# Performance work log

Hardware: AMD Instinct MI355X
Metric: run time of the kernel (lower is better)

The kernel has to match this reference:

```python
import jax, jax.numpy as jnp
import numpy as np

N = 1000000
SH_COEFFS = 16  # (sh_degree+1)^2 with sh_degree=3
H = 256
W = 256
K_RENDER = 1000  # module renders min(1000, N) front-most-by-descending-depth splats


def setup_inputs():
    key = jax.random.key(0)
    k = jax.random.split(key, 5)
    positions = jax.random.normal(k[0], (N, 3), jnp.float32) * 0.1
    scales = jnp.ones((N, 3), jnp.float32) * 0.01
    rotations = jax.random.normal(k[1], (N, 4), jnp.float32)
    colors = jax.random.normal(k[2], (N, 3), jnp.float32)
    opacity = jnp.ones((N, 1), jnp.float32) * 0.1
    colors_sh = jax.random.normal(k[3], (N, SH_COEFFS, 3), jnp.float32) * 0.001
    # realistic pinhole camera: fx=fy=500, cx=cy=128, translation z=2 so depths>0
    camera_matrix = jnp.array([[500.0, 0.0, 128.0, 0.0],
                               [0.0, 500.0, 128.0, 0.0],
                               [0.0, 0.0, 1.0, 2.0]], jnp.float32)
    camera_position = jax.random.normal(k[4], (3,), jnp.float32) * 0.1
    return {"positions": positions, "scales": scales, "rotations": rotations,
            "colors": colors, "opacity": opacity, "colors_sh": colors_sh,
            "camera_matrix": camera_matrix, "camera_position": camera_position,
            "image_height": H, "image_width": W}


def _covariance(scales, rotations):
    # Sigma = R S S^T R^T, quaternion -> rotation matrix
    q = rotations / jnp.linalg.norm(rotations, axis=-1, keepdims=True)
    w, x, y, z = q[:, 0], q[:, 1], q[:, 2], q[:, 3]
    R = jnp.stack([
        jnp.stack([1 - 2 * (y * y + z * z), 2 * (x * y - w * z), 2 * (x * z + w * y)], -1),
        jnp.stack([2 * (x * y + w * z), 1 - 2 * (x * x + z * z), 2 * (y * z - w * x)], -1),
        jnp.stack([2 * (x * z - w * y), 2 * (y * z + w * x), 1 - 2 * (x * x + y * y)], -1)], -2)  # [N,3,3]
    s2 = jnp.clip(scales, 1e-7, None) ** 2
    return jnp.einsum('nij,nj,nkj->nik', R, s2, R)


def _sh_bases(d):
    x, y, z = d[:, 0], d[:, 1], d[:, 2]
    return jnp.stack([
        jnp.full_like(x, 0.28209479177387814),
        -0.48860251190291987 * y, 0.48860251190291987 * z, -0.48860251190291987 * x,
        1.0925484305920792 * x * y, -1.0925484305920792 * y * z,
        0.31539156525252005 * (2 * z * z - x * x - y * y),
        -1.0925484305920792 * x * z, 0.5462742152960396 * (x * x - y * y)], -1)  # [N,9]


def _forward(positions, scales, rotations, colors, opacity, colors_sh,
             camera_matrix, camera_position, image_height, image_width):
    cov3d = _covariance(jnp.exp(scales), rotations)  # [N,3,3]
    # perspective projection
    pos_h = jnp.concatenate([positions, jnp.ones((positions.shape[0], 1), positions.dtype)], -1)
    proj = pos_h @ camera_matrix.T  # [N,3]
    depths = proj[:, 2]
    pos2d = proj[:, :2] / (depths[:, None] + 1e-7)
    fx, fy = camera_matrix[0, 0], camera_matrix[1, 1]
    zero = jnp.zeros_like(depths)
    J = jnp.stack([
        jnp.stack([fx / depths, zero, -fx * pos2d[:, 0] / depths], -1),
        jnp.stack([zero, fy / depths, -fy * pos2d[:, 1] / depths], -1)], -2)  # [N,2,3]
    cov2d = jnp.einsum('nij,njk,nlk->nil', J, cov3d, J)  # [N,2,2]
    # view-dependent color via SH (only first 9 bases, as in the torch loop)
    vd = positions - camera_position[None]
    vd = vd / jnp.linalg.norm(vd, axis=-1, keepdims=True)
    sh = _sh_bases(vd)
    col = jax.nn.sigmoid(colors + jnp.einsum('nkc,nk->nc', colors_sh[:, :sh.shape[-1]], sh))
    op = jax.nn.sigmoid(opacity[:, 0])
    # depth sort descending, keep first K_RENDER (matches min(1000, N) loop)
    order = jnp.argsort(-depths)[:K_RENDER]
    mu_s, cov_s, col_s, op_s = pos2d[order], cov2d[order], col[order], op[order]
    ys = jnp.arange(image_height, dtype=jnp.float32)
    xs = jnp.arange(image_width, dtype=jnp.float32)
    yy, xx = jnp.meshgrid(ys, xs, indexing='ij')
    px = xx.reshape(-1)
    py = yy.reshape(-1)  # [P]
    P = image_height * image_width

    def step(carry, g):
        rendered, acc = carry
        mu, cv, c, o = g
        # 2x2 inverse of (cov + 1e-6 I), closed form
        a = cv[0, 0] + 1e-6
        b = cv[0, 1]
        cc = cv[1, 0]
        d = cv[1, 1] + 1e-6
        det = a * d - b * cc
        dx = px - mu[0]
        dy = py - mu[1]
        qv = (d * dx * dx - (b + cc) * dx * dy + a * dy * dy) / det
        alpha = o * jnp.exp(-0.5 * qv)           # [P]
        contrib = (1.0 - acc) * alpha            # front-to-back compositing
        rendered = rendered + contrib[:, None] * c
        acc = acc + contrib
        return (rendered, acc), None

    init = (jnp.zeros((P, 3), jnp.float32), jnp.zeros((P,), jnp.float32))
    (rendered, _), _ = jax.lax.scan(step, init, (mu_s, cov_s, col_s, op_s))
    return rendered.reshape(image_height, image_width, 3)


def reference(positions, scales, rotations, colors, opacity, colors_sh,
              camera_matrix, camera_position, image_height, image_width):
    return _forward(positions, scales, rotations, colors, opacity, colors_sh,
                    camera_matrix, camera_position, image_height, image_width)
```

## Files before the change

### kernel.cpp

```cpp
#include <hip/hip_runtime.h>
#include <stdint.h>

typedef uint32_t u32;
typedef uint64_t u64;

#define KREN 1000
#define NBLK 256
#define NTHR 1024
#define TOT (NBLK * NTHR)
#define CAND0_CAP 16384
#define CAND_CAP 4096
#define GSTRIDE 12
#define SEGN 16
#define PXT 4

__device__ __forceinline__ u32 fkey(float f) {
  u32 b = __float_as_uint(f);
  return (b & 0x80000000u) ? ~b : (b | 0x80000000u);
}

__device__ __forceinline__ void grid_sync(u32* bar) {
  __syncthreads();
  if (threadIdx.x == 0) {
    u32 gen = __hip_atomic_load(&bar[1], __ATOMIC_RELAXED, __HIP_MEMORY_SCOPE_AGENT);
    u32 arr = __hip_atomic_fetch_add(&bar[0], 1u, __ATOMIC_RELEASE, __HIP_MEMORY_SCOPE_AGENT);
    if (arr == NBLK - 1) {
      __hip_atomic_store(&bar[0], 0u, __ATOMIC_RELAXED, __HIP_MEMORY_SCOPE_AGENT);
      __hip_atomic_store(&bar[1], gen + 1u, __ATOMIC_RELEASE, __HIP_MEMORY_SCOPE_AGENT);
    } else {
      while (__hip_atomic_load(&bar[1], __ATOMIC_RELAXED, __HIP_MEMORY_SCOPE_AGENT) == gen)
        __builtin_amdgcn_s_sleep(4);
    }
    __builtin_amdgcn_fence(__ATOMIC_ACQUIRE, "agent");
  }
  __syncthreads();
}

__device__ __forceinline__ void pick_scan(const u32* __restrict__ hist, u32 K,
                                          u32* lds, int* bin_out, u32* Krem_out) {
  int tid = threadIdx.x;
  u32 hv[4];
  u32 s = 0;
#pragma unroll
  for (int k = 0; k < 4; ++k) { hv[k] = hist[tid * 4 + k]; s += hv[k]; }
  lds[tid] = s;
  __syncthreads();
  for (int d = 1; d < NTHR; d <<= 1) {
    u32 v = lds[tid] + ((tid + d < NTHR) ? lds[tid + d] : 0u);
    __syncthreads();
    lds[tid] = v;
    __syncthreads();
  }
  u32 inc = lds[tid];
  u32 above = (tid < NTHR - 1) ? lds[tid + 1] : 0u;
  if (above < K && inc >= K) {
    u32 cum = above;
    for (int k = 3; k >= 0; --k) {
      cum += hv[k];
      if (cum >= K) {
        lds[NTHR] = (u32)(tid * 4 + k);
        lds[NTHR + 1] = K - (cum - hv[k]);
        break;
      }
    }
  }
  __syncthreads();
  *bin_out = (int)lds[NTHR];
  *Krem_out = lds[NTHR + 1];
  __syncthreads();
}

__global__ __launch_bounds__(NTHR) void k_fused(
    const float* __restrict__ pos, const float* __restrict__ scales,
    const float* __restrict__ rot, const float* __restrict__ colors,
    const float* __restrict__ opac, const float* __restrict__ csh,
    const float* __restrict__ cam, const float* __restrict__ campos,
    u32* __restrict__ keys, u64* __restrict__ cand0, u64* __restrict__ cand,
    float* __restrict__ gauss, u32* __restrict__ hist1, u32* __restrict__ hist2,
    u32* __restrict__ state, u32* __restrict__ bar, float* __restrict__ out,
    int N, int shstride) {
  __shared__ u64 smem[8192];
  u32* hl = (u32*)smem;
  int tid = threadIdx.x, bid = blockIdx.x;
  int gtid = bid * NTHR + tid;
  int lane = tid & 63;

  for (int i = tid; i < 4096; i += NTHR) hl[i] = 0;
  __syncthreads();
  {
    float c8 = cam[8], c9 = cam[9], c10 = cam[10], c11 = cam[11];
    for (int i = gtid; i < N; i += TOT) {
      float x = pos[3 * i], y = pos[3 * i + 1], z = pos[3 * i + 2];
      u32 mk = fkey(c8 * x + c9 * y + c10 * z + c11);
      keys[i] = mk;
      u32 bin = mk >> 20;
      u64 todo = __ballot(true);
      while (todo) {
        int leader = __ffsll((unsigned long long)todo) - 1;
        u32 lbin = __shfl(bin, leader, 64);
        u64 same = __ballot(bin == lbin);
        if (lane == leader) atomicAdd(&hl[lbin], (u32)__popcll(same & todo));
        todo &= ~same;
      }
    }
  }
  __syncthreads();
  for (int i = tid; i < 4096; i += NTHR) {
    u32 v = hl[i];
    if (v) atomicAdd(&hist1[i], v);
  }
  grid_sync(bar);

  int bin1; u32 K1;
  pick_scan(hist1, (u32)KREN, hl, &bin1, &K1);
  u32 pref = (u32)bin1;
  for (int i = tid; i < 4096; i += NTHR) hl[i] = 0;
  __syncthreads();
  for (int i = gtid; i < N; i += TOT) {
    u32 k = keys[i];
    bool m = (k >> 20) == pref;
    if (m) atomicAdd(&hl[(k >> 8) & 4095u], 1u);
    u64 bm = __ballot(m);
    if (bm) {
      u32 base;
      int leader = __ffsll((unsigned long long)bm) - 1;
      if (lane == leader) base = atomicAdd(&state[1], (u32)__popcll(bm));
      base = __shfl(base, leader, 64);
      if (m) {
        u32 p = base + (u32)__popcll(bm & ((1ull << lane) - 1ull));
        if (p < CAND0_CAP) cand0[p] = (((u64)(~k)) << 32) | (u32)i;
      }
    }
  }
  __syncthreads();
  for (int i = tid; i < 4096; i += NTHR) {
    u32 v = hl[i];
    if (v) atomicAdd(&hist2[i], v);
  }
  grid_sync(bar);

  int bin2; u32 K2;
  pick_scan(hist2, K1, hl, &bin2, &K2);
  {
    u32 Thi = ~((pref << 20) | (((u32)bin2) << 8));
    int M1 = (int)state[1];
    if (M1 > CAND0_CAP) M1 = CAND0_CAP;
    for (int i = gtid; i < M1; i += TOT) {
      u64 e = cand0[i];
      if ((u32)(e >> 32) <= Thi) {
        u32 p = atomicAdd(&state[0], 1u);
        if (p < CAND_CAP) cand[p] = e;
      }
    }
  }
  grid_sync(bar);

  {
    u64* sc = smem;
    int M = (int)state[0];
    if (M > CAND_CAP) M = CAND_CAP;
    for (int i = tid; i < M; i += NTHR) sc[i] = cand[i];
    __syncthreads();
    int w = tid >> 6;
    int c = bid * 16 + w;
    if (c < M) {
      u64 mine = sc[c];
      int cnt = 0;
      int JJ = (M + 63) >> 6;
      for (int jj = 0; jj < JJ; ++jj) {
        int j = lane + (jj << 6);
        if (j < M && sc[j] < mine) ++cnt;
      }
#pragma unroll
      for (int d = 32; d; d >>= 1) cnt += __shfl_xor(cnt, d, 64);
      int r = cnt;
      if (r < KREN && lane == 0) {
        int g = (int)(u32)(mine & 0xffffffffu);
        float x = pos[3 * g], y = pos[3 * g + 1], z = pos[3 * g + 2];
        float c0 = cam[0], c1 = cam[1], c2 = cam[2], c3 = cam[3];
        float c4 = cam[4], c5 = cam[5], c6 = cam[6], c7 = cam[7];
        float c8 = cam[8], c9 = cam[9], c10 = cam[10], c11 = cam[11];
        float dep = c8 * x + c9 * y + c10 * z + c11;
        float invd = 1.0f / (dep + 1e-7f);
        float p2x = (c0 * x + c1 * y + c2 * z + c3) * invd;
        float p2y = (c4 * x + c5 * y + c6 * z + c7) * invd;
        float qw = rot[4 * g], qx = rot[4 * g + 1], qy = rot[4 * g + 2], qz = rot[4 * g + 3];
        float qn = rsqrtf(qw * qw + qx * qx + qy * qy + qz * qz);
        qw *= qn; qx *= qn; qy *= qn; qz *= qn;
        float r00 = 1.f - 2.f * (qy * qy + qz * qz), r01 = 2.f * (qx * qy - qw * qz), r02 = 2.f * (qx * qz + qw * qy);
        float r10 = 2.f * (qx * qy + qw * qz), r11 = 1.f - 2.f * (qx * qx + qz * qz), r12 = 2.f * (qy * qz - qw * qx);
        float r20 = 2.f * (qx * qz - qw * qy), r21 = 2.f * (qy * qz + qw * qx), r22 = 1.f - 2.f * (qx * qx + qy * qy);
        float e0 = fmaxf(expf(scales[3 * g]), 1e-7f);
        float e1 = fmaxf(expf(scales[3 * g + 1]), 1e-7f);
        float e2 = fmaxf(expf(scales[3 * g + 2]), 1e-7f);
        float v0 = e0 * e0, v1 = e1 * e1, v2 = e2 * e2;
        float C00 = r00 * r00 * v0 + r01 * r01 * v1 + r02 * r02 * v2;
        float C01 = r00 * r10 * v0 + r01 * r11 * v1 + r02 * r12 * v2;
        float C02 = r00 * r20 * v0 + r01 * r21 * v1 + r02 * r22 * v2;
        float C11 = r10 * r10 * v0 + r11 * r11 * v1 + r12 * r12 * v2;
        float C12 = r10 * r20 * v0 + r11 * r21 * v1 + r12 * r22 * v2;
        float C22 = r20 * r20 * v0 + r21 * r21 * v1 + r22 * r22 * v2;
        float fx = c0, fy = c5;
        float jd = 1.0f / dep;
        float j0 = fx * jd, j2 = -fx * p2x * jd, j4 = fy * jd, j5 = -fy * p2y * jd;
        float u0x = j0 * C00 + j2 * C02;
        float u0y = j0 * C01 + j2 * C12;
        float u0z = j0 * C02 + j2 * C22;
        float u1y = j4 * C11 + j5 * C12;
        float u1z = j4 * C12 + j5 * C22;
        float a = u0x * j0 + u0z * j2 + 1e-6f;
        float b = u0y * j4 + u0z * j5;
        float d2 = u1y * j4 + u1z * j5 + 1e-6f;
        float det = a * d2 - b * b;
        float idet = 1.0f / det;
        const float L = 1.4426950408889634f;
        float Aq = -0.5f * L * d2 * idet;
        float Bq = L * b * idet;
        float Cq = -0.5f * L * a * idet;
        float vx = x - campos[0], vy = y - campos[1], vz = z - campos[2];
        float vn = rsqrtf(vx * vx + vy * vy + vz * vz);
        vx *= vn; vy *= vn; vz *= vn;
        float sh[9];
        sh[0] = 0.28209479177387814f;
        sh[1] = -0.48860251190291987f * vy;
        sh[2] = 0.48860251190291987f * vz;
        sh[3] = -0.48860251190291987f * vx;
        sh[4] = 1.0925484305920792f * vx * vy;
        sh[5] = -1.0925484305920792f * vy * vz;
        sh[6] = 0.31539156525252005f * (2.f * vz * vz - vx * vx - vy * vy);
        sh[7] = -1.0925484305920792f * vx * vz;
        sh[8] = 0.5462742152960396f * (vx * vx - vy * vy);
        float col[3];
        for (int c2 = 0; c2 < 3; ++c2) {
          float accv = colors[3 * g + c2];
          for (int k2 = 0; k2 < 9; ++k2) accv += sh[k2] * csh[(size_t)g * shstride + 3 * k2 + c2];
          col[c2] = 1.0f / (1.0f + __expf(-accv));
        }
        float op = 1.0f / (1.0f + __expf(-opac[g]));
        float* G = gauss + r * GSTRIDE;
        G[0] = p2x; G[1] = p2y; G[2] = Aq; G[3] = Bq; G[4] = Cq;
        G[5] = op;  G[6] = col[0]; G[7] = col[1]; G[8] = col[2];
        G[9] = 0.f; G[10] = 0.f; G[11] = 0.f;
      }
    }
  }
  grid_sync(bar);

  {
    float* gs = (float*)smem;
    float4* g4s = (float4*)smem;
    const float4* g4 = (const float4*)gauss;
    for (int i = tid; i < 3000; i += NTHR) g4s[i] = g4[i];
    __syncthreads();
    int grp = tid & 63;
    int seg = tid >> 6;
    float pxf = (float)(grp * 4);
    float pyf = (float)bid;
    float cr0 = 0.f, cr1 = 0.f, cr2 = 0.f, cr3 = 0.f;
    float cg0 = 0.f, cg1 = 0.f, cg2 = 0.f, cg3 = 0.f;
    float cb0 = 0.f, cb1 = 0.f, cb2 = 0.f, cb3 = 0.f;
    float ac0 = 0.f, ac1 = 0.f, ac2 = 0.f, ac3 = 0.f;
    int gbeg = (seg * KREN) / SEGN, gend = ((seg + 1) * KREN) / SEGN;
    for (int k = gbeg; k < gend; ++k) {
      const float4* Gp = (const float4*)(gs + k * GSTRIDE);
      float4 g0 = Gp[0];
      float4 g1 = Gp[1];
      float g2x = gs[k * GSTRIDE + 8];
      float A = g0.z, B = g0.w, C = g1.x, op = g1.y;
      float dx = pxf - g0.x, dy = pyf - g0.y;
      float q0 = (A * dx + B * dy) * dx + C * dy * dy;
      float u = 2.f * A * dx + B * dy;
      float q1 = q0 + u + A;
      float q2 = q0 + 2.f * u + 4.f * A;
      float q3 = q0 + 3.f * u + 9.f * A;
      float e0 = op * exp2f(q0), e1 = op * exp2f(q1);
      float e2 = op * exp2f(q2), e3 = op * exp2f(q3);
      float w0 = (1.f - ac0) * e0, w1 = (1.f - ac1) * e1;
      float w2 = (1.f - ac2) * e2, w3 = (1.f - ac3) * e3;
      cr0 += w0 * g1.z; cg0 += w0 * g1.w; cb0 += w0 * g2x; ac0 += w0;
      cr1 += w1 * g1.z; cg1 += w1 * g1.w; cb1 += w1 * g2x; ac1 += w1;
      cr2 += w2 * g1.z; cg2 += w2 * g1.w; cb2 += w2 * g2x; ac2 += w2;
      cr3 += w3 * g1.z; cg3 += w3 * g1.w; cb3 += w3 * g2x; ac3 += w3;
    }
    __syncthreads();
    float4* comb = (float4*)smem;
    int base = seg * 256 + grp * 4;
    comb[base + 0] = make_float4(cr0, cg0, cb0, 1.f - ac0);
    comb[base + 1] = make_float4(cr1, cg1, cb1, 1.f - ac1);
    comb[base + 2] = make_float4(cr2, cg2, cb2, 1.f - ac2);
    comb[base + 3] = make_float4(cr3, cg3, cb3, 1.f - ac3);
    __syncthreads();
    if (tid < 256) {
      int px = tid;
      float R = 0.f, Gc = 0.f, Bc = 0.f, T = 1.f;
#pragma unroll
      for (int s2 = 0; s2 < SEGN; ++s2) {
        float4 cv = comb[s2 * 256 + px];
        R += T * cv.x; Gc += T * cv.y; Bc += T * cv.z;
        T *= cv.w;
      }
      int p = bid * 256 + px;
      out[3 * p + 0] = R;
      out[3 * p + 1] = Gc;
      out[3 * p + 2] = Bc;
    }
  }
}

extern "C" void kernel_launch(void* const* d_in, const int* in_sizes, int n_in,
                              void* d_out, int out_size, void* d_ws, size_t ws_size,
                              hipStream_t stream) {
  const float* positions = (const float*)d_in[0];
  const float* scales    = (const float*)d_in[1];
  const float* rotations = (const float*)d_in[2];
  const float* colors    = (const float*)d_in[3];
  const float* opacity   = (const float*)d_in[4];
  const float* colors_sh = (const float*)d_in[5];
  const float* cam       = (const float*)d_in[6];
  const float* campos    = (const float*)d_in[7];
  int N = in_sizes[0] / 3;
  int shstride = in_sizes[5] / N;

  char* ws = (char*)d_ws;
  u32* keys    = (u32*)ws;
  u64* cand0   = (u64*)(ws + 4194304);
  u64* cand    = (u64*)(ws + 4325376);
  float* gauss = (float*)(ws + 4358144);
  char* zr     = ws + 4407296;
  u32* hist1   = (u32*)zr;
  u32* hist2   = (u32*)(zr + 16384);
  u32* state   = (u32*)(zr + 32768);
  u32* bar     = (u32*)(zr + 33024);
  float* out   = (float*)d_out;

  hipMemsetAsync(zr, 0, 33280, stream);

  void* args[] = {(void*)&positions, (void*)&scales, (void*)&rotations, (void*)&colors,
                  (void*)&opacity, (void*)&colors_sh, (void*)&cam, (void*)&campos,
                  (void*)&keys, (void*)&cand0, (void*)&cand, (void*)&gauss,
                  (void*)&hist1, (void*)&hist2, (void*)&state, (void*)&bar,
                  (void*)&out, (void*)&N, (void*)&shstride};
  hipLaunchCooperativeKernel((const void*)k_fused, dim3(NBLK), dim3(NTHR), args, 0, stream);
}
```

Baseline: 450.2 us.

## Split cooperative fused kernel into five stream-ordered kernels

Replaces the single cooperative kernel and its software grid barriers with five separate launches (key/histogram, refine histogram and candidate gather, threshold filter, rank and preprocess, render), each with its own grid and block size. The candidate filter now uses wave-aggregated atomics instead of per-thread atomics, and the first-stage bin and remaining count are passed between kernels through workspace state. This is meant to remove the cost of spinning grid barriers and cooperative launch limits, and to let each phase use a suitable occupancy. In exchange it adds several kernel launch gaps and re-reads intermediate data from global memory.

```diff
diff --git a/kernel.cpp b/kernel.cpp
--- a/kernel.cpp
+++ b/kernel.cpp
@@ -5,118 +5,101 @@
 typedef uint64_t u64;
 
 #define KREN 1000
-#define NBLK 256
-#define NTHR 1024
-#define TOT (NBLK * NTHR)
 #define CAND0_CAP 16384
 #define CAND_CAP 4096
 #define GSTRIDE 12
 #define SEGN 16
-#define PXT 4
+#define P0_BLK 512
+#define P1_BLK 512
+#define P2_BLK 32
+#define P3_BLK 1024
 
 __device__ __forceinline__ u32 fkey(float f) {
   u32 b = __float_as_uint(f);
   return (b & 0x80000000u) ? ~b : (b | 0x80000000u);
 }
 
-__device__ __forceinline__ void grid_sync(u32* bar) {
-  __syncthreads();
-  if (threadIdx.x == 0) {
-    u32 gen = __hip_atomic_load(&bar[1], __ATOMIC_RELAXED, __HIP_MEMORY_SCOPE_AGENT);
-    u32 arr = __hip_atomic_fetch_add(&bar[0], 1u, __ATOMIC_RELEASE, __HIP_MEMORY_SCOPE_AGENT);
-    if (arr == NBLK - 1) {
-      __hip_atomic_store(&bar[0], 0u, __ATOMIC_RELAXED, __HIP_MEMORY_SCOPE_AGENT);
-      __hip_atomic_store(&bar[1], gen + 1u, __ATOMIC_RELEASE, __HIP_MEMORY_SCOPE_AGENT);
-    } else {
-      while (__hip_atomic_load(&bar[1], __ATOMIC_RELAXED, __HIP_MEMORY_SCOPE_AGENT) == gen)
-        __builtin_amdgcn_s_sleep(4);
-    }
-    __builtin_amdgcn_fence(__ATOMIC_ACQUIRE, "agent");
-  }
-  __syncthreads();
-}
-
-__device__ __forceinline__ void pick_scan(const u32* __restrict__ hist, u32 K,
-                                          u32* lds, int* bin_out, u32* Krem_out) {
+__device__ __forceinline__ void pick_scan256(const u32* __restrict__ hist, u32 K,
+                                             u32* lds, int* bin_out, u32* Krem_out) {
   int tid = threadIdx.x;
-  u32 hv[4];
+  u32 hv[16];
   u32 s = 0;
 #pragma unroll
-  for (int k = 0; k < 4; ++k) { hv[k] = hist[tid * 4 + k]; s += hv[k]; }
+  for (int k = 0; k < 16; ++k) { hv[k] = hist[tid * 16 + k]; s += hv[k]; }
   lds[tid] = s;
   __syncthreads();
-  for (int d = 1; d < NTHR; d <<= 1) {
-    u32 v = lds[tid] + ((tid + d < NTHR) ? lds[tid + d] : 0u);
+  for (int d = 1; d < 256; d <<= 1) {
+    u32 v = lds[tid] + ((tid + d < 256) ? lds[tid + d] : 0u);
     __syncthreads();
     lds[tid] = v;
     __syncthreads();
   }
   u32 inc = lds[tid];
-  u32 above = (tid < NTHR - 1) ? lds[tid + 1] : 0u;
+  u32 above = (tid < 255) ? lds[tid + 1] : 0u;
   if (above < K && inc >= K) {
     u32 cum = above;
-    for (int k = 3; k >= 0; --k) {
+    for (int k = 15; k >= 0; --k) {
       cum += hv[k];
       if (cum >= K) {
-        lds[NTHR] = (u32)(tid * 4 + k);
-        lds[NTHR + 1] = K - (cum - hv[k]);
+        lds[256] = (u32)(tid * 16 + k);
+        lds[257] = K - (cum - hv[k]);
         break;
       }
     }
   }
   __syncthreads();
-  *bin_out = (int)lds[NTHR];
-  *Krem_out = lds[NTHR + 1];
-  __syncthreads();
-}
-
-__global__ __launch_bounds__(NTHR) void k_fused(
-    const float* __restrict__ pos, const float* __restrict__ scales,
-    const float* __restrict__ rot, const float* __restrict__ colors,
-    const float* __restrict__ opac, const float* __restrict__ csh,
-    const float* __restrict__ cam, const float* __restrict__ campos,
-    u32* __restrict__ keys, u64* __restrict__ cand0, u64* __restrict__ cand,
-    float* __restrict__ gauss, u32* __restrict__ hist1, u32* __restrict__ hist2,
-    u32* __restrict__ state, u32* __restrict__ bar, float* __restrict__ out,
-    int N, int shstride) {
-  __shared__ u64 smem[8192];
-  u32* hl = (u32*)smem;
-  int tid = threadIdx.x, bid = blockIdx.x;
-  int gtid = bid * NTHR + tid;
+  *bin_out = (int)lds[256];
+  *Krem_out = lds[257];
+  __syncthreads();
+}
+
+__global__ __launch_bounds__(256) void k_p0(const float* __restrict__ pos,
+                                            const float* __restrict__ cam,
+                                            u32* __restrict__ keys,
+                                            u32* __restrict__ hist1, int N) {
+  __shared__ u32 hl[4096];
+  int tid = threadIdx.x;
   int lane = tid & 63;
-
-  for (int i = tid; i < 4096; i += NTHR) hl[i] = 0;
-  __syncthreads();
-  {
-    float c8 = cam[8], c9 = cam[9], c10 = cam[10], c11 = cam[11];
-    for (int i = gtid; i < N; i += TOT) {
-      float x = pos[3 * i], y = pos[3 * i + 1], z = pos[3 * i + 2];
-      u32 mk = fkey(c8 * x + c9 * y + c10 * z + c11);
-      keys[i] = mk;
-      u32 bin = mk >> 20;
-      u64 todo = __ballot(true);
-      while (todo) {
-        int leader = __ffsll((unsigned long long)todo) - 1;
-        u32 lbin = __shfl(bin, leader, 64);
-        u64 same = __ballot(bin == lbin);
-        if (lane == leader) atomicAdd(&hl[lbin], (u32)__popcll(same & todo));
-        todo &= ~same;
-      }
-    }
-  }
-  __syncthreads();
-  for (int i = tid; i < 4096; i += NTHR) {
+  for (int i = tid; i < 4096; i += 256) hl[i] = 0;
+  __syncthreads();
+  float c8 = cam[8], c9 = cam[9], c10 = cam[10], c11 = cam[11];
+  for (int i = blockIdx.x * 256 + tid; i < N; i += P0_BLK * 256) {
+    float x = pos[3 * i], y = pos[3 * i + 1], z = pos[3 * i + 2];
+    u32 mk = fkey(c8 * x + c9 * y + c10 * z + c11);
+    keys[i] = mk;
+    u32 bin = mk >> 20;
+    u64 todo = __ballot(true);
+    while (todo) {
+      int leader = __ffsll((unsigned long long)todo) - 1;
+      u32 lbin = __shfl(bin, leader, 64);
+      u64 same = __ballot(bin == lbin);
+      if (lane == leader) atomicAdd(&hl[lbin], (u32)__popcll(same & todo));
+      todo &= ~same;
+    }
+  }
+  __syncthreads();
+  for (int i = tid; i < 4096; i += 256) {
     u32 v = hl[i];
     if (v) atomicAdd(&hist1[i], v);
   }
-  grid_sync(bar);
-
+}
+
+__global__ __launch_bounds__(256) void k_p1(const u32* __restrict__ keys,
+                                            const u32* __restrict__ hist1,
+                                            u32* __restrict__ hist2,
+                                            u64* __restrict__ cand0,
+                                            u32* __restrict__ state, int N) {
+  __shared__ u32 hl[4096];
+  __shared__ u32 sl[258];
+  int tid = threadIdx.x;
+  int lane = tid & 63;
   int bin1; u32 K1;
-  pick_scan(hist1, (u32)KREN, hl, &bin1, &K1);
+  pick_scan256(hist1, (u32)KREN, sl, &bin1, &K1);
+  if (tid == 0) { state[4] = K1; state[5] = (u32)bin1; }
   u32 pref = (u32)bin1;
-  for (int i = tid; i < 4096; i += NTHR) hl[i] = 0;
-  __syncthreads();
-  for (int i = gtid; i < N; i += TOT) {
+  for (int i = tid; i < 4096; i += 256) hl[i] = 0;
+  __syncthreads();
+  for (int i = blockIdx.x * 256 + tid; i < N; i += P1_BLK * 256) {
     u32 k = keys[i];
     bool m = (k >> 20) == pref;
     if (m) atomicAdd(&hl[(k >> 8) & 4095u], 1u);
@@ -133,177 +116,199 @@
     }
   }
   __syncthreads();
-  for (int i = tid; i < 4096; i += NTHR) {
+  for (int i = tid; i < 4096; i += 256) {
     u32 v = hl[i];
     if (v) atomicAdd(&hist2[i], v);
   }
-  grid_sync(bar);
-
+}
+
+__global__ __launch_bounds__(256) void k_p2(const u64* __restrict__ cand0,
+                                            const u32* __restrict__ hist2,
+                                            u64* __restrict__ cand,
+                                            u32* __restrict__ state) {
+  __shared__ u32 sl[258];
+  int tid = threadIdx.x;
+  int lane = tid & 63;
+  u32 K1 = state[4];
+  u32 pref = state[5];
   int bin2; u32 K2;
-  pick_scan(hist2, K1, hl, &bin2, &K2);
-  {
-    u32 Thi = ~((pref << 20) | (((u32)bin2) << 8));
-    int M1 = (int)state[1];
-    if (M1 > CAND0_CAP) M1 = CAND0_CAP;
-    for (int i = gtid; i < M1; i += TOT) {
-      u64 e = cand0[i];
-      if ((u32)(e >> 32) <= Thi) {
-        u32 p = atomicAdd(&state[0], 1u);
+  pick_scan256(hist2, K1, sl, &bin2, &K2);
+  u32 Thi = ~((pref << 20) | (((u32)bin2) << 8));
+  int M1 = (int)state[1];
+  if (M1 > CAND0_CAP) M1 = CAND0_CAP;
+  for (int i = blockIdx.x * 256 + tid; i < M1; i += P2_BLK * 256) {
+    u64 e = cand0[i];
+    bool m = (u32)(e >> 32) <= Thi;
+    u64 bm = __ballot(m);
+    if (bm) {
+      u32 base;
+      int leader = __ffsll((unsigned long long)bm) - 1;
+      if (lane == leader) base = atomicAdd(&state[0], (u32)__popcll(bm));
+      base = __shfl(base, leader, 64);
+      if (m) {
+        u32 p = base + (u32)__popcll(bm & ((1ull << lane) - 1ull));
         if (p < CAND_CAP) cand[p] = e;
       }
     }
   }
-  grid_sync(bar);
-
-  {
-    u64* sc = smem;
-    int M = (int)state[0];
-    if (M > CAND_CAP) M = CAND_CAP;
-    for (int i = tid; i < M; i += NTHR) sc[i] = cand[i];
-    __syncthreads();
-    int w = tid >> 6;
-    int c = bid * 16 + w;
-    if (c < M) {
-      u64 mine = sc[c];
-      int cnt = 0;
-      int JJ = (M + 63) >> 6;
-      for (int jj = 0; jj < JJ; ++jj) {
-        int j = lane + (jj << 6);
-        if (j < M && sc[j] < mine) ++cnt;
-      }
+}
+
+__global__ __launch_bounds__(256) void k_p3(
+    const u64* __restrict__ cand, const u32* __restrict__ state,
+    const float* __restrict__ pos, const float* __restrict__ scales,
+    const float* __restrict__ rot, const float* __restrict__ colors,
+    const float* __restrict__ opac, const float* __restrict__ csh,
+    const float* __restrict__ cam, const float* __restrict__ campos,
+    float* __restrict__ gauss, int shstride) {
+  __shared__ u64 sc[CAND_CAP];
+  int tid = threadIdx.x, bid = blockIdx.x;
+  int lane = tid & 63;
+  int M = (int)state[0];
+  if (M > CAND_CAP) M = CAND_CAP;
+  if (bid * 4 >= M) return;
+  for (int i = tid; i < M; i += 256) sc[i] = cand[i];
+  __syncthreads();
+  int c = bid * 4 + (tid >> 6);
+  if (c >= M) return;
+  u64 mine = sc[c];
+  int cnt = 0;
+  int JJ = (M + 63) >> 6;
+  for (int jj = 0; jj < JJ; ++jj) {
+    int j = lane + (jj << 6);
+    if (j < M && sc[j] < mine) ++cnt;
+  }
 #pragma unroll
-      for (int d = 32; d; d >>= 1) cnt += __shfl_xor(cnt, d, 64);
-      int r = cnt;
-      if (r < KREN && lane == 0) {
-        int g = (int)(u32)(mine & 0xffffffffu);
-        float x = pos[3 * g], y = pos[3 * g + 1], z = pos[3 * g + 2];
-        float c0 = cam[0], c1 = cam[1], c2 = cam[2], c3 = cam[3];
-        float c4 = cam[4], c5 = cam[5], c6 = cam[6], c7 = cam[7];
-        float c8 = cam[8], c9 = cam[9], c10 = cam[10], c11 = cam[11];
-        float dep = c8 * x + c9 * y + c10 * z + c11;
-        float invd = 1.0f / (dep + 1e-7f);
-        float p2x = (c0 * x + c1 * y + c2 * z + c3) * invd;
-        float p2y = (c4 * x + c5 * y + c6 * z + c7) * invd;
-        float qw = rot[4 * g], qx = rot[4 * g + 1], qy = rot[4 * g + 2], qz = rot[4 * g + 3];
-        float qn = rsqrtf(qw * qw + qx * qx + qy * qy + qz * qz);
-        qw *= qn; qx *= qn; qy *= qn; qz *= qn;
-        float r00 = 1.f - 2.f * (qy * qy + qz * qz), r01 = 2.f * (qx * qy - qw * qz), r02 = 2.f * (qx * qz + qw * qy);
-        float r10 = 2.f * (qx * qy + qw * qz), r11 = 1.f - 2.f * (qx * qx + qz * qz), r12 = 2.f * (qy * qz - qw * qx);
-        float r20 = 2.f * (qx * qz - qw * qy), r21 = 2.f * (qy * qz + qw * qx), r22 = 1.f - 2.f * (qx * qx + qy * qy);
-        float e0 = fmaxf(expf(scales[3 * g]), 1e-7f);
-        float e1 = fmaxf(expf(scales[3 * g + 1]), 1e-7f);
-        float e2 = fmaxf(expf(scales[3 * g + 2]), 1e-7f);
-        float v0 = e0 * e0, v1 = e1 * e1, v2 = e2 * e2;
-        float C00 = r00 * r00 * v0 + r01 * r01 * v1 + r02 * r02 * v2;
-        float C01 = r00 * r10 * v0 + r01 * r11 * v1 + r02 * r12 * v2;
-        float C02 = r00 * r20 * v0 + r01 * r21 * v1 + r02 * r22 * v2;
-        float C11 = r10 * r10 * v0 + r11 * r11 * v1 + r12 * r12 * v2;
-        float C12 = r10 * r20 * v0 + r11 * r21 * v1 + r12 * r22 * v2;
-        float C22 = r20 * r20 * v0 + r21 * r21 * v1 + r22 * r22 * v2;
-        float fx = c0, fy = c5;
-        float jd = 1.0f / dep;
-        float j0 = fx * jd, j2 = -fx * p2x * jd, j4 = fy * jd, j5 = -fy * p2y * jd;
-        float u0x = j0 * C00 + j2 * C02;
-        float u0y = j0 * C01 + j2 * C12;
-        float u0z = j0 * C02 + j2 * C22;
-        float u1y = j4 * C11 + j5 * C12;
-        float u1z = j4 * C12 + j5 * C22;
-        float a = u0x * j0 + u0z * j2 + 1e-6f;
-        float b = u0y * j4 + u0z * j5;
-        float d2 = u1y * j4 + u1z * j5 + 1e-6f;
-        float det = a * d2 - b * b;
-        float idet = 1.0f / det;
-        const float L = 1.4426950408889634f;
-        float Aq = -0.5f * L * d2 * idet;
-        float Bq = L * b * idet;
-        float Cq = -0.5f * L * a * idet;
-        float vx = x - campos[0], vy = y - campos[1], vz = z - campos[2];
-        float vn = rsqrtf(vx * vx + vy * vy + vz * vz);
-        vx *= vn; vy *= vn; vz *= vn;
-        float sh[9];
-        sh[0] = 0.28209479177387814f;
-        sh[1] = -0.48860251190291987f * vy;
-        sh[2] = 0.48860251190291987f * vz;
-        sh[3] = -0.48860251190291987f * vx;
-        sh[4] = 1.0925484305920792f * vx * vy;
-        sh[5] = -1.0925484305920792f * vy * vz;
-        sh[6] = 0.31539156525252005f * (2.f * vz * vz - vx * vx - vy * vy);
-        sh[7] = -1.0925484305920792f * vx * vz;
-        sh[8] = 0.5462742152960396f * (vx * vx - vy * vy);
-        float col[3];
-        for (int c2 = 0; c2 < 3; ++c2) {
-          float accv = colors[3 * g + c2];
-          for (int k2 = 0; k2 < 9; ++k2) accv += sh[k2] * csh[(size_t)g * shstride + 3 * k2 + c2];
-          col[c2] = 1.0f / (1.0f + __expf(-accv));
-        }
-        float op = 1.0f / (1.0f + __expf(-opac[g]));
-        float* G = gauss + r * GSTRIDE;
-        G[0] = p2x; G[1] = p2y; G[2] = Aq; G[3] = Bq; G[4] = Cq;
-        G[5] = op;  G[6] = col[0]; G[7] = col[1]; G[8] = col[2];
-        G[9] = 0.f; G[10] = 0.f; G[11] = 0.f;
-      }
-    }
-  }
-  grid_sync(bar);
-
-  {
-    float* gs = (float*)smem;
-    float4* g4s = (float4*)smem;
-    const float4* g4 = (const float4*)gauss;
-    for (int i = tid; i < 3000; i += NTHR) g4s[i] = g4[i];
-    __syncthreads();
-    int grp = tid & 63;
-    int seg = tid >> 6;
-    float pxf = (float)(grp * 4);
-    float pyf = (float)bid;
-    float cr0 = 0.f, cr1 = 0.f, cr2 = 0.f, cr3 = 0.f;
-    float cg0 = 0.f, cg1 = 0.f, cg2 = 0.f, cg3 = 0.f;
-    float cb0 = 0.f, cb1 = 0.f, cb2 = 0.f, cb3 = 0.f;
-    float ac0 = 0.f, ac1 = 0.f, ac2 = 0.f, ac3 = 0.f;
-    int gbeg = (seg * KREN) / SEGN, gend = ((seg + 1) * KREN) / SEGN;
-    for (int k = gbeg; k < gend; ++k) {
-      const float4* Gp = (const float4*)(gs + k * GSTRIDE);
-      float4 g0 = Gp[0];
-      float4 g1 = Gp[1];
-      float g2x = gs[k * GSTRIDE + 8];
-      float A = g0.z, B = g0.w, C = g1.x, op = g1.y;
-      float dx = pxf - g0.x, dy = pyf - g0.y;
-      float q0 = (A * dx + B * dy) * dx + C * dy * dy;
-      float u = 2.f * A * dx + B * dy;
-      float q1 = q0 + u + A;
-      float q2 = q0 + 2.f * u + 4.f * A;
-      float q3 = q0 + 3.f * u + 9.f * A;
-      float e0 = op * exp2f(q0), e1 = op * exp2f(q1);
-      float e2 = op * exp2f(q2), e3 = op * exp2f(q3);
-      float w0 = (1.f - ac0) * e0, w1 = (1.f - ac1) * e1;
-      float w2 = (1.f - ac2) * e2, w3 = (1.f - ac3) * e3;
-      cr0 += w0 * g1.z; cg0 += w0 * g1.w; cb0 += w0 * g2x; ac0 += w0;
-      cr1 += w1 * g1.z; cg1 += w1 * g1.w; cb1 += w1 * g2x; ac1 += w1;
-      cr2 += w2 * g1.z; cg2 += w2 * g1.w; cb2 += w2 * g2x; ac2 += w2;
-      cr3 += w3 * g1.z; cg3 += w3 * g1.w; cb3 += w3 * g2x; ac3 += w3;
-    }
-    __syncthreads();
-    float4* comb = (float4*)smem;
-    int base = seg * 256 + grp * 4;
-    comb[base + 0] = make_float4(cr0, cg0, cb0, 1.f - ac0);
-    comb[base + 1] = make_float4(cr1, cg1, cb1, 1.f - ac1);
-    comb[base + 2] = make_float4(cr2, cg2, cb2, 1.f - ac2);
-    comb[base + 3] = make_float4(cr3, cg3, cb3, 1.f - ac3);
-    __syncthreads();
-    if (tid < 256) {
-      int px = tid;
-      float R = 0.f, Gc = 0.f, Bc = 0.f, T = 1.f;
+  for (int d = 32; d; d >>= 1) cnt += __shfl_xor(cnt, d, 64);
+  int r = cnt;
+  if (r >= KREN || lane != 0) return;
+  int g = (int)(u32)(mine & 0xffffffffu);
+  float x = pos[3 * g], y = pos[3 * g + 1], z = pos[3 * g + 2];
+  float c0 = cam[0], c1 = cam[1], c2 = cam[2], c3 = cam[3];
+  float c4 = cam[4], c5 = cam[5], c6 = cam[6], c7 = cam[7];
+  float c8 = cam[8], c9 = cam[9], c10 = cam[10], c11 = cam[11];
+  float dep = c8 * x + c9 * y + c10 * z + c11;
+  float invd = 1.0f / (dep + 1e-7f);
+  float p2x = (c0 * x + c1 * y + c2 * z + c3) * invd;
+  float p2y = (c4 * x + c5 * y + c6 * z + c7) * invd;
+  float qw = rot[4 * g], qx = rot[4 * g + 1], qy = rot[4 * g + 2], qz = rot[4 * g + 3];
+  float qn = rsqrtf(qw * qw + qx * qx + qy * qy + qz * qz);
+  qw *= qn; qx *= qn; qy *= qn; qz *= qn;
+  float r00 = 1.f - 2.f * (qy * qy + qz * qz), r01 = 2.f * (qx * qy - qw * qz), r02 = 2.f * (qx * qz + qw * qy);
+  float r10 = 2.f * (qx * qy + qw * qz), r11 = 1.f - 2.f * (qx * qx + qz * qz), r12 = 2.f * (qy * qz - qw * qx);
+  float r20 = 2.f * (qx * qz - qw * qy), r21 = 2.f * (qy * qz + qw * qx), r22 = 1.f - 2.f * (qx * qx + qy * qy);
+  float e0 = fmaxf(expf(scales[3 * g]), 1e-7f);
+  float e1 = fmaxf(expf(scales[3 * g + 1]), 1e-7f);
+  float e2 = fmaxf(expf(scales[3 * g + 2]), 1e-7f);
+  float v0 = e0 * e0, v1 = e1 * e1, v2 = e2 * e2;
+  float C00 = r00 * r00 * v0 + r01 * r01 * v1 + r02 * r02 * v2;
+  float C01 = r00 * r10 * v0 + r01 * r11 * v1 + r02 * r12 * v2;
+  float C02 = r00 * r20 * v0 + r01 * r21 * v1 + r02 * r22 * v2;
+  float C11 = r10 * r10 * v0 + r11 * r11 * v1 + r12 * r12 * v2;
+  float C12 = r10 * r20 * v0 + r11 * r21 * v1 + r12 * r22 * v2;
+  float C22 = r20 * r20 * v0 + r21 * r21 * v1 + r22 * r22 * v2;
+  float fx = c0, fy = c5;
+  float jd = 1.0f / dep;
+  float j0 = fx * jd, j2 = -fx * p2x * jd, j4 = fy * jd, j5 = -fy * p2y * jd;
+  float u0x = j0 * C00 + j2 * C02;
+  float u0y = j0 * C01 + j2 * C12;
+  float u0z = j0 * C02 + j2 * C22;
+  float u1y = j4 * C11 + j5 * C12;
+  float u1z = j4 * C12 + j5 * C22;
+  float a = u0x * j0 + u0z * j2 + 1e-6f;
+  float b = u0y * j4 + u0z * j5;
+  float d2 = u1y * j4 + u1z * j5 + 1e-6f;
+  float det = a * d2 - b * b;
+  float idet = 1.0f / det;
+  const float L = 1.4426950408889634f;
+  float Aq = -0.5f * L * d2 * idet;
+  float Bq = L * b * idet;
+  float Cq = -0.5f * L * a * idet;
+  float vx = x - campos[0], vy = y - campos[1], vz = z - campos[2];
+  float vn = rsqrtf(vx * vx + vy * vy + vz * vz);
+  vx *= vn; vy *= vn; vz *= vn;
+  float sh[9];
+  sh[0] = 0.28209479177387814f;
+  sh[1] = -0.48860251190291987f * vy;
+  sh[2] = 0.48860251190291987f * vz;
+  sh[3] = -0.48860251190291987f * vx;
+  sh[4] = 1.0925484305920792f * vx * vy;
+  sh[5] = -1.0925484305920792f * vy * vz;
+  sh[6] = 0.31539156525252005f * (2.f * vz * vz - vx * vx - vy * vy);
+  sh[7] = -1.0925484305920792f * vx * vz;
+  sh[8] = 0.5462742152960396f * (vx * vx - vy * vy);
+  float col[3];
+  for (int c2 = 0; c2 < 3; ++c2) {
+    float accv = colors[3 * g + c2];
+    for (int k2 = 0; k2 < 9; ++k2) accv += sh[k2] * csh[(size_t)g * shstride + 3 * k2 + c2];
+    col[c2] = 1.0f / (1.0f + __expf(-accv));
+  }
+  float op = 1.0f / (1.0f + __expf(-opac[g]));
+  float* G = gauss + r * GSTRIDE;
+  G[0] = p2x; G[1] = p2y; G[2] = Aq; G[3] = Bq; G[4] = Cq;
+  G[5] = op;  G[6] = col[0]; G[7] = col[1]; G[8] = col[2];
+  G[9] = 0.f; G[10] = 0.f; G[11] = 0.f;
+}
+
+__global__ __launch_bounds__(1024) void k_p4(const float* __restrict__ gauss,
+                                             float* __restrict__ out) {
+  __shared__ u64 smem[8192];
+  int tid = threadIdx.x, bid = blockIdx.x;
+  float* gs = (float*)smem;
+  float4* g4s = (float4*)smem;
+  const float4* g4 = (const float4*)gauss;
+  for (int i = tid; i < 3000; i += 1024) g4s[i] = g4[i];
+  __syncthreads();
+  int grp = tid & 63;
+  int seg = tid >> 6;
+  float pxf = (float)(grp * 4);
+  float pyf = (float)bid;
+  float cr0 = 0.f, cr1 = 0.f, cr2 = 0.f, cr3 = 0.f;
+  float cg0 = 0.f, cg1 = 0.f, cg2 = 0.f, cg3 = 0.f;
+  float cb0 = 0.f, cb1 = 0.f, cb2 = 0.f, cb3 = 0.f;
+  float ac0 = 0.f, ac1 = 0.f, ac2 = 0.f, ac3 = 0.f;
+  int gbeg = (seg * KREN) / SEGN, gend = ((seg + 1) * KREN) / SEGN;
+  for (int k = gbeg; k < gend; ++k) {
+    const float4* Gp = (const float4*)(gs + k * GSTRIDE);
+    float4 g0 = Gp[0];
+    float4 g1 = Gp[1];
+    float g2x = gs[k * GSTRIDE + 8];
+    float A = g0.z, B = g0.w, C = g1.x, op = g1.y;
+    float dx = pxf - g0.x, dy = pyf - g0.y;
+    float q0 = (A * dx + B * dy) * dx + C * dy * dy;
+    float u = 2.f * A * dx + B * dy;
+    float q1 = q0 + u + A;
+    float q2 = q0 + 2.f * u + 4.f * A;
+    float q3 = q0 + 3.f * u + 9.f * A;
+    float e0 = op * exp2f(q0), e1 = op * exp2f(q1);
+    float e2 = op * exp2f(q2), e3 = op * exp2f(q3);
+    float w0 = (1.f - ac0) * e0, w1 = (1.f - ac1) * e1;
+    float w2 = (1.f - ac2) * e2, w3 = (1.f - ac3) * e3;
+    cr0 += w0 * g1.z; cg0 += w0 * g1.w; cb0 += w0 * g2x; ac0 += w0;
+    cr1 += w1 * g1.z; cg1 += w1 * g1.w; cb1 += w1 * g2x; ac1 += w1;
+    cr2 += w2 * g1.z; cg2 += w2 * g1.w; cb2 += w2 * g2x; ac2 += w2;
+    cr3 += w3 * g1.z; cg3 += w3 * g1.w; cb3 += w3 * g2x; ac3 += w3;
+  }
+  __syncthreads();
+  float4* comb = (float4*)smem;
+  int base = seg * 256 + grp * 4;
+  comb[base + 0] = make_float4(cr0, cg0, cb0, 1.f - ac0);
+  comb[base + 1] = make_float4(cr1, cg1, cb1, 1.f - ac1);
+  comb[base + 2] = make_float4(cr2, cg2, cb2, 1.f - ac2);
+  comb[base + 3] = make_float4(cr3, cg3, cb3, 1.f - ac3);
+  __syncthreads();
+  if (tid < 256) {
+    int px = tid;
+    float R = 0.f, Gc = 0.f, Bc = 0.f, T = 1.f;
 #pragma unroll
-      for (int s2 = 0; s2 < SEGN; ++s2) {
-        float4 cv = comb[s2 * 256 + px];
-        R += T * cv.x; Gc += T * cv.y; Bc += T * cv.z;
-        T *= cv.w;
-      }
-      int p = bid * 256 + px;
-      out[3 * p + 0] = R;
-      out[3 * p + 1] = Gc;
-      out[3 * p + 2] = Bc;
-    }
+    for (int s2 = 0; s2 < SEGN; ++s2) {
+      float4 cv = comb[s2 * 256 + px];
+      R += T * cv.x; Gc += T * cv.y; Bc += T * cv.z;
+      T *= cv.w;
+    }
+    int p = bid * 256 + px;
+    out[3 * p + 0] = R;
+    out[3 * p + 1] = Gc;
+    out[3 * p + 2] = Bc;
   }
 }
 
@@ -330,15 +335,14 @@
   u32* hist1   = (u32*)zr;
   u32* hist2   = (u32*)(zr + 16384);
   u32* state   = (u32*)(zr + 32768);
-  u32* bar     = (u32*)(zr + 33024);
   float* out   = (float*)d_out;
 
   hipMemsetAsync(zr, 0, 33280, stream);
-
-  void* args[] = {(void*)&positions, (void*)&scales, (void*)&rotations, (void*)&colors,
-                  (void*)&opacity, (void*)&colors_sh, (void*)&cam, (void*)&campos,
-                  (void*)&keys, (void*)&cand0, (void*)&cand, (void*)&gauss,
-                  (void*)&hist1, (void*)&hist2, (void*)&state, (void*)&bar,
-                  (void*)&out, (void*)&N, (void*)&shstride};
-  hipLaunchCooperativeKernel((const void*)k_fused, dim3(NBLK), dim3(NTHR), args, 0, stream);
-}
+  k_p0<<<P0_BLK, 256, 0, stream>>>(positions, cam, keys, hist1, N);
+  k_p1<<<P1_BLK, 256, 0, stream>>>(keys, hist1, hist2, cand0, state, N);
+  k_p2<<<P2_BLK, 256, 0, stream>>>(cand0, hist2, cand, state);
+  k_p3<<<P3_BLK, 256, 0, stream>>>(cand, state, positions, scales, rotations,
+                                   colors, opacity, colors_sh, cam, campos,
+                                   gauss, shstride);
+  k_p4<<<256, 1024, 0, stream>>>(gauss, out);
+}
```

Measured after the change: 378.1 us. -16.0%, faster.
